# Kernel tuning notes

Measured on AMD Instinct MI355X. Metric: run time of the kernel, lower is better.

The kernel has to match this reference:

```python
import jax, jax.numpy as jnp
import numpy as np

N = 50000      # nodes
E = 800000     # edges
D = 128        # node feature dim
H = 128        # hid_channel (hardcoded in module)
B = 64         # graphs in batch
C = 3          # num_classes (COLLAB)
K = N // 2     # TopKPooling ratio=0.5


def setup_inputs() -> dict:
    key = jax.random.key(0)
    ks = jax.random.split(key, 16)
    s = 0.05
    return {
        "x": jax.random.normal(ks[0], (N, D), dtype=jnp.float32),
        "edge_index": jax.random.randint(ks[1], (E, 2), 0, N),
        "batch": jnp.sort(jax.random.randint(ks[2], (N,), 0, B)),
        "W1": jax.random.normal(ks[3], (D, H), dtype=jnp.float32) * s,
        "b1": jnp.zeros((H,), jnp.float32),
        "W2": jax.random.normal(ks[4], (H, H), dtype=jnp.float32) * s,
        "b2": jnp.zeros((H,), jnp.float32),
        "p": jax.random.normal(ks[5], (H,), dtype=jnp.float32),
        "W3": jax.random.normal(ks[6], (H, H), dtype=jnp.float32) * s,
        "b3": jnp.zeros((H,), jnp.float32),
        "W4": jax.random.normal(ks[7], (H, H), dtype=jnp.float32) * s,
        "b4": jnp.zeros((H,), jnp.float32),
        "fcW1": jax.random.normal(ks[8], (H, H), dtype=jnp.float32) * s,
        "fcb1": jnp.zeros((H,), jnp.float32),
        "fcW2": jax.random.normal(ks[9], (H, C), dtype=jnp.float32) * s,
        "fcb2": jnp.zeros((C,), jnp.float32),
    }


def gcn_conv(x, src, dst, ew, W, b, n):
    # PyG GCNConv: D^{-1/2}(A+I)D^{-1/2} x W + b, deg includes self-loop
    h = x @ W
    deg = jax.ops.segment_sum(ew, dst, num_segments=n) + 1.0
    dinv = jax.lax.rsqrt(deg)
    coef = dinv[src] * dinv[dst] * ew            # [E]
    agg = jax.ops.segment_sum(coef[:, None] * h[src], dst, num_segments=n)
    return agg + (dinv * dinv)[:, None] * h + b  # self-loop term + bias


def reference(x, edge_index, batch, W1, b1, W2, b2, p, W3, b3, W4, b4, fcW1, fcb1, fcW2, fcb2):
    src, dst = edge_index[:, 0], edge_index[:, 1]
    ew = jnp.ones((E,), x.dtype)

    h = jax.nn.relu(gcn_conv(x, src, dst, ew, W1, b1, N))
    h = jax.nn.relu(gcn_conv(h, src, dst, ew, W2, b2, N))

    # TopKPooling: score = x.p/||p||, keep top K, gate by tanh(score)
    score = h @ p / jnp.linalg.norm(p)
    top_vals, perm = jax.lax.top_k(score, K)
    hp = h[perm] * jnp.tanh(top_vals)[:, None]
    batch_p = batch[perm]
    new_idx = jnp.full((N,), -1, jnp.int32).at[perm].set(jnp.arange(K, dtype=jnp.int32))
    ns, nd = new_idx[src], new_idx[dst]
    mask = (ns >= 0) & (nd >= 0)
    ewp = mask.astype(x.dtype)
    ns = jnp.where(mask, ns, 0)
    nd = jnp.where(mask, nd, 0)

    h = jax.nn.relu(gcn_conv(hp, ns, nd, ewp, W3, b3, K))
    h = jax.nn.relu(gcn_conv(h, ns, nd, ewp, W4, b4, K))

    # global mean pool over graphs
    sums = jax.ops.segment_sum(h, batch_p, num_segments=B)
    cnt = jax.ops.segment_sum(jnp.ones((K,), x.dtype), batch_p, num_segments=B)
    g = sums / jnp.maximum(cnt, 1.0)[:, None]

    g = jax.nn.relu(g @ fcW1 + fcb1)
    logits = g @ fcW2 + fcb2
    return jax.nn.log_softmax(logits, axis=1)
```

## Files before the change

### kernel.cpp

```cpp
#include <hip/hip_runtime.h>

#define N_NODES 50000
#define N_EDGES 800000
#define HDIM    128
#define NBATCH  64
#define NCLS    3
#define KSEL    (N_NODES/2)
#define MMB_ROWS 64
#define HIST_BLOCKS 128
#define POOL_BLOCKS 256
#define POOL_CHUNK  ((KSEL + POOL_BLOCKS - 1) / POOL_BLOCKS)
#define NBUCK ((N_NODES + 127) >> 7)
#define EPB   2048
#define S1_BLOCKS ((N_EDGES + EPB - 1) / EPB)
#define SEG_CAP 4096

typedef unsigned long long u64;
typedef unsigned int u32;
typedef unsigned short ushort_t;
typedef _Float16 half8 __attribute__((ext_vector_type(8)));
typedef float floatx4 __attribute__((ext_vector_type(4)));

struct SelState { u64 prefix; int krem; int cnt; };

__device__ __forceinline__ float h2f(ushort_t u) {
    _Float16 h = *(_Float16*)&u;
    return (float)h;
}

__global__ void init_pnorm_k(const float* __restrict__ p, float* __restrict__ pn,
        SelState* st) {
    __shared__ float red[HDIM];
    int t = threadIdx.x;
    float v = p[t];
    red[t] = v * v;
    __syncthreads();
    for (int s = HDIM/2; s > 0; s >>= 1) {
        if (t < s) red[t] += red[t+s];
        __syncthreads();
    }
    pn[t] = v / sqrtf(red[0]);
    if (t == 0) { st->prefix = 0ull; st->krem = KSEL; st->cnt = 0; }
}

__global__ void deg_full_k(const int* __restrict__ ei, int* __restrict__ degi) {
    int e = blockIdx.x * blockDim.x + threadIdx.x;
    if (e >= N_EDGES) return;
    int2 ed = ((const int2*)ei)[e];
    atomicAdd(&degi[ed.y], 1);
}

__global__ __launch_bounds__(256) void scan12_k(const int* __restrict__ degi,
        int* __restrict__ bsum, int* __restrict__ boff, float* __restrict__ dinv,
        int* __restrict__ rowptr, int n, int nb, int* done) {
    __shared__ int sh[256];
    __shared__ int lastf;
    int t = threadIdx.x;
    int i = blockIdx.x * 256 + t;
    int d = (i < n) ? degi[i] : 0;
    if (i < n) dinv[i] = rsqrtf((float)d + 1.0f);
    sh[t] = d;
    __syncthreads();
    for (int s = 128; s > 0; s >>= 1) {
        if (t < s) sh[t] += sh[t + s];
        __syncthreads();
    }
    if (t == 0) {
        atomicExch(&bsum[blockIdx.x], sh[0]);
        __threadfence();
        int dd = atomicAdd(done, 1);
        lastf = (dd == (int)gridDim.x - 1) ? 1 : 0;
    }
    __syncthreads();
    if (lastf) {
        int v = (t < nb) ? atomicAdd(&bsum[t], 0) : 0;
        sh[t] = v;
        __syncthreads();
        for (int dl = 1; dl < 256; dl <<= 1) {
            int u = (t >= dl) ? sh[t - dl] : 0;
            __syncthreads();
            sh[t] += u;
            __syncthreads();
        }
        if (t < nb) boff[t] = sh[t] - v;
        if (t == 255) rowptr[n] = sh[255];
    }
}

__global__ __launch_bounds__(256) void scan3_k(const int* __restrict__ degi,
        const int* __restrict__ boff, int* __restrict__ rowptr, int n) {
    __shared__ int sh[256];
    int t = threadIdx.x;
    int i = blockIdx.x * 256 + t;
    int v = (i < n) ? degi[i] : 0;
    sh[t] = v;
    __syncthreads();
    for (int d = 1; d < 256; d <<= 1) {
        int u = (t >= d) ? sh[t - d] : 0;
        __syncthreads();
        sh[t] += u;
        __syncthreads();
    }
    if (i < n) rowptr[i] = boff[blockIdx.x] + sh[t] - v;
}

__global__ __launch_bounds__(256) void csr_bucket_k(const int* __restrict__ ei,
        const int* __restrict__ rowptr, u32* __restrict__ gcnt, u32* __restrict__ ebuf) {
    __shared__ u32 bh[NBUCK];
    __shared__ u32 cursor[NBUCK];
    int t = threadIdx.x;
    for (int i = t; i < NBUCK; i += 256) bh[i] = 0;
    __syncthreads();
    int e0 = blockIdx.x * EPB;
    int2 ed[8]; int nb[8];
#pragma unroll
    for (int i = 0; i < 8; ++i) {
        int e = e0 + t + i * 256;
        if (e < N_EDGES) {
            ed[i] = ((const int2*)ei)[e];
            nb[i] = ed[i].y >> 7;
            atomicAdd(&bh[nb[i]], 1u);
        } else nb[i] = -1;
    }
    __syncthreads();
    for (int b = t; b < NBUCK; b += 256) {
        u32 c = bh[b];
        if (c) cursor[b] = (u32)rowptr[b << 7] + atomicAdd(&gcnt[b], c);
    }
    __syncthreads();
#pragma unroll
    for (int i = 0; i < 8; ++i) {
        if (nb[i] >= 0) {
            u32 pos = atomicAdd(&cursor[nb[i]], 1u);
            ebuf[pos] = ((u32)(ed[i].y & 127) << 16) | (u32)ed[i].x;
        }
    }
}

__global__ __launch_bounds__(256) void csr_build_k(const u32* __restrict__ ebuf,
        const int* __restrict__ rowptr, int* __restrict__ csr) {
    __shared__ int rp[129];
    __shared__ int fcnt[128];
    __shared__ int seg[SEG_CAP];
    int b = blockIdx.x;
    int lo = b << 7;
    int nn = min(128, N_NODES - lo);
    int t = threadIdx.x;
    if (t <= nn) rp[t] = rowptr[lo + t];
    if (t < 128) fcnt[t] = 0;
    __syncthreads();
    int segbase = rp[0];
    int segsz = rp[nn] - segbase;
    if (segsz <= SEG_CAP) {
        for (int idx = t; idx < segsz; idx += 256) {
            u32 v = ebuf[segbase + idx];
            int dl = v >> 16;
            int slot = rp[dl] - segbase + atomicAdd(&fcnt[dl], 1);
            seg[slot] = (int)(v & 0xFFFFu);
        }
        __syncthreads();
        for (int idx = t; idx < segsz; idx += 256) csr[segbase + idx] = seg[idx];
    } else {
        for (int idx = t; idx < segsz; idx += 256) {
            u32 v = ebuf[segbase + idx];
            int dl = v >> 16;
            int slot = rp[dl] + atomicAdd(&fcnt[dl], 1);
            csr[slot] = (int)(v & 0xFFFFu);
        }
    }
}

__global__ __launch_bounds__(256) void gather_k(const int* __restrict__ rowptr,
        const int* __restrict__ csr, const float* __restrict__ dinv,
        const ushort_t* __restrict__ hb, const float* __restrict__ bias,
        float* __restrict__ out, int n) {
    int node = blockIdx.x * 4 + (threadIdx.x >> 6);
    if (node >= n) return;
    int lane = threadIdx.x & 63;
    float di = dinv[node];
    float2 bv = *(const float2*)&bias[2*lane];
    ushort2 hs = *(const ushort2*)&hb[(size_t)node * HDIM + 2*lane];
    float s2 = di * di;
    float accx = s2 * h2f(hs.x) + bv.x;
    float accy = s2 * h2f(hs.y) + bv.y;
    int rs = rowptr[node], re = rowptr[node + 1];
    for (int base = rs; base < re; base += 64) {
        int cnt = min(64, re - base);
        int srcv = 0; float cv = 0.0f;
        if (lane < cnt) { srcv = csr[base + lane]; cv = di * dinv[srcv]; }
        int j = 0;
        for (; j + 8 <= cnt; j += 8) {
            int s0 = __shfl(srcv, j+0, 64); int s1 = __shfl(srcv, j+1, 64);
            int s2i= __shfl(srcv, j+2, 64); int s3 = __shfl(srcv, j+3, 64);
            int s4 = __shfl(srcv, j+4, 64); int s5 = __shfl(srcv, j+5, 64);
            int s6 = __shfl(srcv, j+6, 64); int s7 = __shfl(srcv, j+7, 64);
            float c0 = __shfl(cv, j+0, 64); float c1 = __shfl(cv, j+1, 64);
            float c2 = __shfl(cv, j+2, 64); float c3 = __shfl(cv, j+3, 64);
            float c4 = __shfl(cv, j+4, 64); float c5 = __shfl(cv, j+5, 64);
            float c6 = __shfl(cv, j+6, 64); float c7 = __shfl(cv, j+7, 64);
            ushort2 v0 = *(const ushort2*)&hb[(size_t)s0 * HDIM + 2*lane];
            ushort2 v1 = *(const ushort2*)&hb[(size_t)s1 * HDIM + 2*lane];
            ushort2 v2 = *(const ushort2*)&hb[(size_t)s2i* HDIM + 2*lane];
            ushort2 v3 = *(const ushort2*)&hb[(size_t)s3 * HDIM + 2*lane];
            ushort2 v4 = *(const ushort2*)&hb[(size_t)s4 * HDIM + 2*lane];
            ushort2 v5 = *(const ushort2*)&hb[(size_t)s5 * HDIM + 2*lane];
            ushort2 v6 = *(const ushort2*)&hb[(size_t)s6 * HDIM + 2*lane];
            ushort2 v7 = *(const ushort2*)&hb[(size_t)s7 * HDIM + 2*lane];
            accx += c0*h2f(v0.x); accy += c0*h2f(v0.y);
            accx += c1*h2f(v1.x); accy += c1*h2f(v1.y);
            accx += c2*h2f(v2.x); accy += c2*h2f(v2.y);
            accx += c3*h2f(v3.x); accy += c3*h2f(v3.y);
            accx += c4*h2f(v4.x); accy += c4*h2f(v4.y);
            accx += c5*h2f(v5.x); accy += c5*h2f(v5.y);
            accx += c6*h2f(v6.x); accy += c6*h2f(v6.y);
            accx += c7*h2f(v7.x); accy += c7*h2f(v7.y);
        }
        for (; j < cnt; ++j) {
            int src = __shfl(srcv, j, 64);
            float c  = __shfl(cv, j, 64);
            ushort2 sv = *(const ushort2*)&hb[(size_t)src * HDIM + 2*lane];
            accx += c * h2f(sv.x);
            accy += c * h2f(sv.y);
        }
    }
    float2 o; o.x = accx; o.y = accy;
    *(float2*)&out[(size_t)node * HDIM + 2*lane] = o;
}

__global__ __launch_bounds__(256) void gather_pool_k(const int* __restrict__ rowptr,
        const int* __restrict__ csr, const int* __restrict__ n2o,
        const int2* __restrict__ pinfo, const float* __restrict__ dinvp,
        const ushort_t* __restrict__ hb, const float* __restrict__ bias,
        float* __restrict__ out) {
    __shared__ int   sns[4][64];
    __shared__ float scf[4][64];
    int k = blockIdx.x * 4 + (threadIdx.x >> 6);
    if (k >= KSEL) return;
    int wid = threadIdx.x >> 6, lane = threadIdx.x & 63;
    float di = dinvp[k];
    float2 bv = *(const float2*)&bias[2*lane];
    ushort2 hs = *(const ushort2*)&hb[(size_t)k * HDIM + 2*lane];
    float s2 = di * di;
    float accx = s2 * h2f(hs.x) + bv.x;
    float accy = s2 * h2f(hs.y) + bv.y;
    int old = n2o[k];
    int rs = rowptr[old], re = rowptr[old + 1];
    for (int base = rs; base < re; base += 64) {
        int span = min(64, re - base);
        int ns = -1; float dv = 0.0f;
        if (lane < span) {
            int2 pi = pinfo[csr[base + lane]];
            ns = pi.x; dv = __int_as_float(pi.y);
        }
        bool sel = (ns >= 0);
        u64 m = __ballot(sel);
        int rank = __popcll(m & ((1ull << lane) - 1ull));
        if (sel) { sns[wid][rank] = ns; scf[wid][rank] = di * dv; }
        int cnt = __popcll(m);
        __threadfence_block();
        int j = 0;
        for (; j + 8 <= cnt; j += 8) {
            int s0 = sns[wid][j+0]; int s1 = sns[wid][j+1];
            int s2i= sns[wid][j+2]; int s3 = sns[wid][j+3];
            int s4 = sns[wid][j+4]; int s5 = sns[wid][j+5];
            int s6 = sns[wid][j+6]; int s7 = sns[wid][j+7];
            float c0 = scf[wid][j+0]; float c1 = scf[wid][j+1];
            float c2 = scf[wid][j+2]; float c3 = scf[wid][j+3];
            float c4 = scf[wid][j+4]; float c5 = scf[wid][j+5];
            float c6 = scf[wid][j+6]; float c7 = scf[wid][j+7];
            ushort2 v0 = *(const ushort2*)&hb[(size_t)s0 * HDIM + 2*lane];
            ushort2 v1 = *(const ushort2*)&hb[(size_t)s1 * HDIM + 2*lane];
            ushort2 v2 = *(const ushort2*)&hb[(size_t)s2i* HDIM + 2*lane];
            ushort2 v3 = *(const ushort2*)&hb[(size_t)s3 * HDIM + 2*lane];
            ushort2 v4 = *(const ushort2*)&hb[(size_t)s4 * HDIM + 2*lane];
            ushort2 v5 = *(const ushort2*)&hb[(size_t)s5 * HDIM + 2*lane];
            ushort2 v6 = *(const ushort2*)&hb[(size_t)s6 * HDIM + 2*lane];
            ushort2 v7 = *(const ushort2*)&hb[(size_t)s7 * HDIM + 2*lane];
            accx += c0*h2f(v0.x); accy += c0*h2f(v0.y);
            accx += c1*h2f(v1.x); accy += c1*h2f(v1.y);
            accx += c2*h2f(v2.x); accy += c2*h2f(v2.y);
            accx += c3*h2f(v3.x); accy += c3*h2f(v3.y);
            accx += c4*h2f(v4.x); accy += c4*h2f(v4.y);
            accx += c5*h2f(v5.x); accy += c5*h2f(v5.y);
            accx += c6*h2f(v6.x); accy += c6*h2f(v6.y);
            accx += c7*h2f(v7.x); accy += c7*h2f(v7.y);
        }
        for (; j < cnt; ++j) {
            int src = sns[wid][j];
            float c = scf[wid][j];
            ushort2 sv = *(const ushort2*)&hb[(size_t)src * HDIM + 2*lane];
            accx += c * h2f(sv.x);
            accy += c * h2f(sv.y);
        }
    }
    float2 o; o.x = accx; o.y = accy;
    *(float2*)&out[(size_t)k * HDIM + 2*lane] = o;
}

template<bool RELU_IN>
__global__ __launch_bounds__(256) void matmul_k(const float* __restrict__ in,
        const float* __restrict__ W, ushort_t* __restrict__ outb, int rows) {
    __shared__ _Float16 Wf[4][8][64][8];
    int t = threadIdx.x;
    int rbase = blockIdx.x * MMB_ROWS;
    for (int idx = t; idx < HDIM * HDIM; idx += 256) {
        int k = idx >> 7, j = idx & 127;
        int kk = k >> 5, kgrp = (k >> 3) & 3, i = k & 7;
        int ct = j >> 4, lrow = j & 15;
        Wf[kk][ct][kgrp * 16 + lrow][i] = (_Float16)W[idx];
    }
    int wid = t >> 6, lane = t & 63;
    int lrow = lane & 15, kgrp = lane >> 4;
    int arow = rbase + wid * 16 + lrow;
    bool rowok = (arow < rows);
    const float* arp = in + (size_t)(rowok ? arow : 0) * HDIM + kgrp * 8;
    half8 a[4];
#pragma unroll
    for (int kk = 0; kk < 4; ++kk) {
        float4 lo = rowok ? *(const float4*)(arp + kk * 32)     : float4{0,0,0,0};
        float4 hi = rowok ? *(const float4*)(arp + kk * 32 + 4) : float4{0,0,0,0};
        if (RELU_IN) {
            lo.x = fmaxf(lo.x, 0.f); lo.y = fmaxf(lo.y, 0.f);
            lo.z = fmaxf(lo.z, 0.f); lo.w = fmaxf(lo.w, 0.f);
            hi.x = fmaxf(hi.x, 0.f); hi.y = fmaxf(hi.y, 0.f);
            hi.z = fmaxf(hi.z, 0.f); hi.w = fmaxf(hi.w, 0.f);
        }
        a[kk][0] = (_Float16)lo.x; a[kk][1] = (_Float16)lo.y;
        a[kk][2] = (_Float16)lo.z; a[kk][3] = (_Float16)lo.w;
        a[kk][4] = (_Float16)hi.x; a[kk][5] = (_Float16)hi.y;
        a[kk][6] = (_Float16)hi.z; a[kk][7] = (_Float16)hi.w;
    }
    __syncthreads();
    floatx4 zero4 = {0.0f, 0.0f, 0.0f, 0.0f};
    floatx4 acc[8];
#pragma unroll
    for (int ct = 0; ct < 8; ++ct) acc[ct] = zero4;
#pragma unroll
    for (int kk = 0; kk < 4; ++kk) {
#pragma unroll
        for (int ct = 0; ct < 8; ++ct) {
            half8 b = *(const half8*)&Wf[kk][ct][lane][0];
            acc[ct] = __builtin_amdgcn_mfma_f32_16x16x32_f16(a[kk], b, acc[ct], 0, 0, 0);
        }
    }
    int orow0 = rbase + wid * 16 + kgrp * 4;
#pragma unroll
    for (int ct = 0; ct < 8; ++ct) {
#pragma unroll
        for (int i = 0; i < 4; ++i) {
            int row = orow0 + i;
            if (row < rows) {
                _Float16 hv = (_Float16)acc[ct][i];
                outb[(size_t)row * HDIM + ct * 16 + lrow] = *(ushort_t*)&hv;
            }
        }
    }
}

__global__ void score_key_k(const float* __restrict__ h, const float* __restrict__ pn,
        float* __restrict__ score, u64* __restrict__ key) {
    int gid  = blockIdx.x * blockDim.x + threadIdx.x;
    int node = gid >> 6;
    int lane = gid & 63;
    if (node >= N_NODES) return;
    const float* row = h + (size_t)node * HDIM;
    float sv = fmaxf(row[lane], 0.f) * pn[lane] + fmaxf(row[lane+64], 0.f) * pn[lane+64];
#pragma unroll
    for (int o = 32; o > 0; o >>= 1) sv += __shfl_xor(sv, o, 64);
    if (lane == 0) {
        score[node] = sv;
        u32 u = __float_as_uint(sv);
        u = (u & 0x80000000u) ? ~u : (u | 0x80000000u);
        key[node] = ((u64)u << 16) | (u64)(65535 - node);
    }
}

__global__ __launch_bounds__(256) void histscan_k(const u64* __restrict__ key,
        SelState* st, u32* __restrict__ hist, int pass, int* done) {
    __shared__ u32 lh[256];
    __shared__ int lastf;
    int t = threadIdx.x;
    lh[t] = 0;
    __syncthreads();
    int dsh = 40 - 8 * pass;
    u64 pref = st->prefix;
    for (int i = blockIdx.x * 256 + t; i < N_NODES; i += HIST_BLOCKS * 256) {
        u64 k = key[i];
        if (((k ^ pref) >> (dsh + 8)) == 0)
            atomicAdd(&lh[(int)((k >> dsh) & 255)], 1u);
    }
    __syncthreads();
    u32 v = lh[t];
    if (v) atomicAdd(&hist[pass * 256 + t], v);
    __threadfence();
    __syncthreads();
    if (t == 0) {
        int dd = atomicAdd(done, 1);
        lastf = (dd == HIST_BLOCKS - 1) ? 1 : 0;
    }
    __syncthreads();
    if (lastf) {
        lh[t] = atomicAdd(&hist[pass * 256 + t], 0u);
        __syncthreads();
        if (t == 0) {
            int krem = st->krem;
            int b = 255;
            for (; b > 0; --b) {
                int cnt = (int)lh[b];
                if (cnt < krem) krem -= cnt;
                else break;
            }
            st->prefix |= ((u64)b) << dsh;
            st->krem = krem;
        }
    }
}

__global__ void select_k(const u64* __restrict__ key, SelState* st,
        int2* __restrict__ pinfo, int* __restrict__ n2o) {
    int i = blockIdx.x * blockDim.x + threadIdx.x;
    if (i >= N_NODES) return;
    if (key[i] >= st->prefix) {
        int pos = atomicAdd(&st->cnt, 1);
        pinfo[i].x = pos;
        n2o[pos] = i;
    } else {
        pinfo[i].x = -1;
    }
}

__global__ void hp_k(const float* __restrict__ h2, const float* __restrict__ score,
        const int* __restrict__ n2o, float* __restrict__ hp) {
    int gid = blockIdx.x * blockDim.x + threadIdx.x;
    if (gid >= KSEL * 32) return;
    int k  = gid >> 5;
    int c4 = (gid & 31) << 2;
    int old = n2o[k];
    float tv = tanhf(score[old]);
    float4 hv = *(const float4*)&h2[(size_t)old * HDIM + c4];
    float4 o;
    o.x = fmaxf(hv.x, 0.f) * tv;
    o.y = fmaxf(hv.y, 0.f) * tv;
    o.z = fmaxf(hv.z, 0.f) * tv;
    o.w = fmaxf(hv.w, 0.f) * tv;
    *(float4*)&hp[(size_t)k * HDIM + c4] = o;
}

__global__ __launch_bounds__(256) void pool_deg_k(const int* __restrict__ rowptr,
        const int* __restrict__ csr, const int* __restrict__ n2o,
        int2* __restrict__ pinfo, float* __restrict__ dinvp) {
    int k = blockIdx.x * 4 + (threadIdx.x >> 6);
    if (k >= KSEL) return;
    int lane = threadIdx.x & 63;
    int old = n2o[k];
    int rs = rowptr[old], re = rowptr[old + 1];
    int cnt = 0;
    for (int base = rs; base < re; base += 64) {
        int span = min(64, re - base);
        bool sel = false;
        if (lane < span) sel = (pinfo[csr[base + lane]].x >= 0);
        cnt += __popcll(__ballot(sel));
    }
    if (lane == 0) {
        float dv = rsqrtf((float)cnt + 1.0f);
        dinvp[k] = dv;
        pinfo[old].y = __float_as_int(dv);
    }
}

__global__ __launch_bounds__(256) void pool_stage1_k(const float* __restrict__ h,
        const int* __restrict__ n2o, const int* __restrict__ batch,
        float* __restrict__ partial, int* __restrict__ pcnt) {
    __shared__ float ls[NBATCH * HDIM];
    __shared__ int   lc[NBATCH];
    int t = threadIdx.x;
    for (int i = t; i < NBATCH * HDIM; i += 256) ls[i] = 0.0f;
    if (t < NBATCH) lc[t] = 0;
    __syncthreads();
    int wid = t >> 6, lane = t & 63;
    int start = blockIdx.x * POOL_CHUNK;
    int end = min(start + POOL_CHUNK, KSEL);
    for (int k = start + wid; k < end; k += 4) {
        int b = batch[n2o[k]];
        float2 hv = *(const float2*)&h[(size_t)k * HDIM + 2*lane];
        atomicAdd(&ls[b * HDIM + 2*lane],     fmaxf(hv.x, 0.0f));
        atomicAdd(&ls[b * HDIM + 2*lane + 1], fmaxf(hv.y, 0.0f));
        if (lane == 0) atomicAdd(&lc[b], 1);
    }
    __syncthreads();
    float* pb = partial + (size_t)blockIdx.x * (NBATCH * HDIM);
    for (int i = t; i < NBATCH * HDIM; i += 256) pb[i] = ls[i];
    if (t < NBATCH) pcnt[blockIdx.x * NBATCH + t] = lc[t];
}

__global__ __launch_bounds__(256) void pool_stage2_k(const float* __restrict__ partial,
        const int* __restrict__ pcnt, float* __restrict__ sums, float* __restrict__ cntb) {
    int i = blockIdx.x * 256 + threadIdx.x;
    if (i >= NBATCH * HDIM) return;
    float s = 0.0f;
    for (int p = 0; p < POOL_BLOCKS; ++p) s += partial[(size_t)p * NBATCH * HDIM + i];
    sums[i] = s;
    if (i < NBATCH) {
        int c = 0;
        for (int p = 0; p < POOL_BLOCKS; ++p) c += pcnt[p * NBATCH + i];
        cntb[i] = (float)c;
    }
}

__global__ void fc1_k(const float* __restrict__ sums, const float* __restrict__ cntb,
        const float* __restrict__ W, const float* __restrict__ bias, float* __restrict__ g) {
    int gid = blockIdx.x * blockDim.x + threadIdx.x;
    if (gid >= NBATCH * HDIM) return;
    int b = gid >> 7, j = gid & 127;
    float inv = 1.0f / fmaxf(cntb[b], 1.0f);
    float acc = 0.0f;
    for (int k = 0; k < HDIM; ++k) acc += sums[b * HDIM + k] * W[k * HDIM + j];
    acc = acc * inv + bias[j];
    g[gid] = fmaxf(acc, 0.0f);
}

__global__ void fc2_k(const float* __restrict__ g, const float* __restrict__ W,
        const float* __restrict__ bias, float* __restrict__ out) {
    int b = threadIdx.x;
    if (b >= NBATCH) return;
    float l[NCLS];
    for (int c = 0; c < NCLS; ++c) {
        float acc = bias[c];
        for (int k = 0; k < HDIM; ++k) acc += g[b * HDIM + k] * W[k * NCLS + c];
        l[c] = acc;
    }
    float m = fmaxf(l[0], fmaxf(l[1], l[2]));
    float sum = expf(l[0]-m) + expf(l[1]-m) + expf(l[2]-m);
    float ls = logf(sum);
    for (int c = 0; c < NCLS; ++c) out[b * NCLS + c] = l[c] - m - ls;
}

extern "C" void kernel_launch(void* const* d_in, const int* in_sizes, int n_in,
                              void* d_out, int out_size, void* d_ws, size_t ws_size,
                              hipStream_t stream) {
    const float* x    = (const float*)d_in[0];
    const int*   ei   = (const int*)d_in[1];
    const int*   batch= (const int*)d_in[2];
    const float* W1   = (const float*)d_in[3];
    const float* b1   = (const float*)d_in[4];
    const float* W2   = (const float*)d_in[5];
    const float* b2   = (const float*)d_in[6];
    const float* p    = (const float*)d_in[7];
    const float* W3   = (const float*)d_in[8];
    const float* b3   = (const float*)d_in[9];
    const float* W4   = (const float*)d_in[10];
    const float* b4   = (const float*)d_in[11];
    const float* fcW1 = (const float*)d_in[12];
    const float* fcb1 = (const float*)d_in[13];
    const float* fcW2 = (const float*)d_in[14];
    const float* fcb2 = (const float*)d_in[15];
    float* out = (float*)d_out;

    char* ws = (char*)d_ws;
    size_t off = 0;
    auto alloc = [&](size_t bytes) {
        size_t r = off;
        off = (off + bytes + 255) & ~(size_t)255;
        return r;
    };
    float* A     = (float*)(ws + alloc((size_t)N_NODES * HDIM * 4));
    float* Bf    = (float*)(ws + alloc((size_t)N_NODES * HDIM * 4));
    ushort_t* Hbf= (ushort_t*)(ws + alloc((size_t)N_NODES * HDIM * 2));
    u64*   key   = (u64*)  (ws + alloc((size_t)N_NODES * 8));
    float* score = (float*)(ws + alloc((size_t)N_NODES * 4));
    int2*  pinfo = (int2*) (ws + alloc((size_t)N_NODES * 8));
    int*   n2o   = (int*)  (ws + alloc((size_t)KSEL * 4));
    float* pn    = (float*)(ws + alloc(HDIM * 4));
    float* gbuf  = (float*)(ws + alloc(NBATCH * HDIM * 4));
    SelState* st = (SelState*)(ws + alloc(256));
    float* dinv1 = (float*)(ws + alloc((size_t)N_NODES * 4));
    float* dinvp = (float*)(ws + alloc((size_t)KSEL * 4));
    int*   rowptr= (int*)  (ws + alloc((size_t)(N_NODES + 1) * 4));
    int*   csr   = (int*)  (ws + alloc((size_t)N_EDGES * 4));
    u32*   ebuf  = (u32*)  (ws + alloc((size_t)N_EDGES * 4));
    int*   bsum  = (int*)  (ws + alloc(256 * 4));
    int*   boff  = (int*)  (ws + alloc(256 * 4));
    float* partial=(float*)(ws + alloc((size_t)POOL_BLOCKS * NBATCH * HDIM * 4));
    int*   pcnt  = (int*)  (ws + alloc((size_t)POOL_BLOCKS * NBATCH * 4));
    float* sums  = (float*)(ws + alloc(NBATCH * HDIM * 4));
    float* cntb  = (float*)(ws + alloc(NBATCH * 4));
    size_t z1 = off;
    int*   degi  = (int*)(ws + alloc((size_t)N_NODES * 4));
    u32*   gcnt  = (u32*)(ws + alloc((size_t)NBUCK * 4));
    u32*   hist  = (u32*)(ws + alloc(6 * 256 * 4));
    int*   done  = (int*)(ws + alloc(16 * 4));
    size_t z1e = off;

    hipMemsetAsync(ws + z1, 0, z1e - z1, stream);
    init_pnorm_k<<<1, HDIM, 0, stream>>>(p, pn, st);

    const int eg   = (N_EDGES + 255) / 256;
    const int ng   = (N_NODES + 255) / 256;
    const int mm_grid_n = (N_NODES + MMB_ROWS - 1) / MMB_ROWS;
    const int mm_grid_k = (KSEL + MMB_ROWS - 1) / MMB_ROWS;
    const int gt_grid_n = (N_NODES + 3) / 4;
    const int gt_grid_k = (KSEL + 3) / 4;
    const int kh4_grid  = (KSEL * 32 + 255) / 256;

    deg_full_k<<<eg, 256, 0, stream>>>(ei, degi);
    scan12_k<<<ng, 256, 0, stream>>>(degi, bsum, boff, dinv1, rowptr, N_NODES, ng, done + 0);
    scan3_k<<<ng, 256, 0, stream>>>(degi, boff, rowptr, N_NODES);
    csr_bucket_k<<<S1_BLOCKS, 256, 0, stream>>>(ei, rowptr, gcnt, ebuf);
    csr_build_k<<<NBUCK, 256, 0, stream>>>(ebuf, rowptr, csr);

    matmul_k<false><<<mm_grid_n, 256, 0, stream>>>(x, W1, Hbf, N_NODES);
    gather_k<<<gt_grid_n, 256, 0, stream>>>(rowptr, csr, dinv1, Hbf, b1, Bf, N_NODES);
    matmul_k<true><<<mm_grid_n, 256, 0, stream>>>(Bf, W2, Hbf, N_NODES);
    gather_k<<<gt_grid_n, 256, 0, stream>>>(rowptr, csr, dinv1, Hbf, b2, Bf, N_NODES);

    score_key_k<<<(N_NODES * 64 + 255) / 256, 256, 0, stream>>>(Bf, pn, score, key);
    for (int pass = 0; pass < 6; ++pass)
        histscan_k<<<HIST_BLOCKS, 256, 0, stream>>>(key, st, hist, pass, done + 2 + pass);
    select_k<<<ng, 256, 0, stream>>>(key, st, pinfo, n2o);
    hp_k<<<kh4_grid, 256, 0, stream>>>(Bf, score, n2o, A);

    pool_deg_k<<<gt_grid_k, 256, 0, stream>>>(rowptr, csr, n2o, pinfo, dinvp);

    matmul_k<false><<<mm_grid_k, 256, 0, stream>>>(A, W3, Hbf, KSEL);
    gather_pool_k<<<gt_grid_k, 256, 0, stream>>>(rowptr, csr, n2o, pinfo, dinvp, Hbf, b3, Bf);
    matmul_k<true><<<mm_grid_k, 256, 0, stream>>>(Bf, W4, Hbf, KSEL);
    gather_pool_k<<<gt_grid_k, 256, 0, stream>>>(rowptr, csr, n2o, pinfo, dinvp, Hbf, b4, A);

    pool_stage1_k<<<POOL_BLOCKS, 256, 0, stream>>>(A, n2o, batch, partial, pcnt);
    pool_stage2_k<<<(NBATCH * HDIM + 255) / 256, 256, 0, stream>>>(partial, pcnt, sums, cntb);
    fc1_k<<<(NBATCH * HDIM + 255) / 256, 256, 0, stream>>>(sums, cntb, fcW1, fcb1, gbuf);
    fc2_k<<<1, 64, 0, stream>>>(gbuf, fcW2, fcb2, out);
}
```

Measured before the change: 422.0 us.

## Fuse top-k selection pipeline into one persistent kernel with grid barriers

Replaces score, six radix histogram passes, select, hp gather and pooled-degree kernels with a single 128-block persistent kernel that uses atomic spin grid barriers between phases. The radix select now uses 12-bit digits over four passes, with a parallel prefix scan over the 4096-bin histogram. fc1 and fc2 are merged using a last-block-done pattern. This removes about ten kernel launches and their launch gaps. In exchange, the later phases run on only 128 blocks, and the spin barriers require every block to be co-resident on the GPU.

```diff
diff --git a/kernel.cpp b/kernel.cpp
--- a/kernel.cpp
+++ b/kernel.cpp
@@ -7,7 +7,7 @@
 #define NCLS    3
 #define KSEL    (N_NODES/2)
 #define MMB_ROWS 64
-#define HIST_BLOCKS 128
+#define TK_BLOCKS 128
 #define POOL_BLOCKS 256
 #define POOL_CHUNK  ((KSEL + POOL_BLOCKS - 1) / POOL_BLOCKS)
 #define NBUCK ((N_NODES + 127) >> 7)
@@ -357,114 +357,148 @@
     }
 }
 
-__global__ void score_key_k(const float* __restrict__ h, const float* __restrict__ pn,
-        float* __restrict__ score, u64* __restrict__ key) {
-    int gid  = blockIdx.x * blockDim.x + threadIdx.x;
-    int node = gid >> 6;
-    int lane = gid & 63;
-    if (node >= N_NODES) return;
-    const float* row = h + (size_t)node * HDIM;
-    float sv = fmaxf(row[lane], 0.f) * pn[lane] + fmaxf(row[lane+64], 0.f) * pn[lane+64];
-#pragma unroll
-    for (int o = 32; o > 0; o >>= 1) sv += __shfl_xor(sv, o, 64);
-    if (lane == 0) {
-        score[node] = sv;
-        u32 u = __float_as_uint(sv);
-        u = (u & 0x80000000u) ? ~u : (u | 0x80000000u);
-        key[node] = ((u64)u << 16) | (u64)(65535 - node);
-    }
-}
-
-__global__ __launch_bounds__(256) void histscan_k(const u64* __restrict__ key,
-        SelState* st, u32* __restrict__ hist, int pass, int* done) {
-    __shared__ u32 lh[256];
+__global__ __launch_bounds__(256) void topk_fused_k(const float* __restrict__ h,
+        const float* __restrict__ pn, float* __restrict__ score, u64* __restrict__ key,
+        SelState* st, u32* __restrict__ ghist, int* __restrict__ sync,
+        int2* __restrict__ pinfo, int* __restrict__ n2o,
+        const int* __restrict__ rowptr, const int* __restrict__ csr,
+        float* __restrict__ dinvp, float* __restrict__ hp) {
+    __shared__ u32 lh[4096];
+    __shared__ u32 sct[256];
+    __shared__ u64 spref;
+    __shared__ int skrem;
     __shared__ int lastf;
     int t = threadIdx.x;
-    lh[t] = 0;
-    __syncthreads();
-    int dsh = 40 - 8 * pass;
-    u64 pref = st->prefix;
-    for (int i = blockIdx.x * 256 + t; i < N_NODES; i += HIST_BLOCKS * 256) {
-        u64 k = key[i];
-        if (((k ^ pref) >> (dsh + 8)) == 0)
-            atomicAdd(&lh[(int)((k >> dsh) & 255)], 1u);
-    }
-    __syncthreads();
-    u32 v = lh[t];
-    if (v) atomicAdd(&hist[pass * 256 + t], v);
+    int lane = t & 63;
+    int gw = blockIdx.x * 4 + (t >> 6);
+
+    float pnl = pn[lane], pnh = pn[lane + 64];
+    for (int node = gw; node < N_NODES; node += TK_BLOCKS * 4) {
+        const float* row = h + (size_t)node * HDIM;
+        float sv = fmaxf(row[lane], 0.f) * pnl + fmaxf(row[lane+64], 0.f) * pnh;
+#pragma unroll
+        for (int o = 32; o > 0; o >>= 1) sv += __shfl_xor(sv, o, 64);
+        if (lane == 0) {
+            score[node] = sv;
+            u32 u = __float_as_uint(sv);
+            u = (u & 0x80000000u) ? ~u : (u | 0x80000000u);
+            key[node] = ((u64)u << 16) | (u64)(65535 - node);
+        }
+    }
+    __syncthreads();
+    if (t == 0) {
+        __threadfence();
+        int v = atomicAdd(&sync[10], 1);
+        if (v == TK_BLOCKS - 1) atomicExch(&sync[11], 1);
+        else while (atomicAdd(&sync[11], 0) == 0) __builtin_amdgcn_s_sleep(8);
+    }
+    __syncthreads();
     __threadfence();
+
+    for (int pass = 0; pass < 4; ++pass) {
+        int dsh = 36 - 12 * pass;
+        if (t == 0) spref = atomicAdd((unsigned long long*)&st->prefix, 0ull);
+        __syncthreads();
+        u64 pref = spref;
+        for (int b = t; b < 4096; b += 256) lh[b] = 0;
+        __syncthreads();
+        for (int i = blockIdx.x * 256 + t; i < N_NODES; i += TK_BLOCKS * 256) {
+            u64 k = key[i];
+            if (((k ^ pref) >> (dsh + 12)) == 0)
+                atomicAdd(&lh[(int)((k >> dsh) & 4095)], 1u);
+        }
+        __syncthreads();
+        for (int b = t; b < 4096; b += 256) {
+            u32 v = lh[b];
+            if (v) atomicAdd(&ghist[pass * 4096 + b], v);
+        }
+        __threadfence();
+        if (t == 0) {
+            int v = atomicAdd(&sync[2 + pass], 1);
+            lastf = (v == TK_BLOCKS - 1) ? 1 : 0;
+        }
+        __syncthreads();
+        if (lastf) {
+            for (int b = t; b < 4096; b += 256) lh[b] = atomicAdd(&ghist[pass * 4096 + b], 0u);
+            if (t == 0) skrem = atomicAdd(&st->krem, 0);
+            __syncthreads();
+            int krem = skrem;
+            u32 ctt = 0;
+#pragma unroll
+            for (int j = 0; j < 16; ++j) ctt += lh[t * 16 + j];
+            sct[t] = ctt;
+            __syncthreads();
+            for (int d = 1; d < 256; d <<= 1) {
+                u32 add = (t + d < 256) ? sct[t + d] : 0u;
+                __syncthreads();
+                sct[t] += add;
+                __syncthreads();
+            }
+            u32 incl = sct[t];
+            u32 excl = incl - ctt;
+            if ((int)excl < krem && (int)incl >= krem) {
+                u32 run = excl;
+                int bsel = 0; u32 csel = 0;
+                for (int j = 15; j >= 0; --j) {
+                    u32 c = lh[t * 16 + j];
+                    run += c;
+                    if ((int)run >= krem) { bsel = t * 16 + j; csel = c; break; }
+                }
+                int newk = krem - (int)(run - csel);
+                atomicExch((unsigned long long*)&st->prefix, spref | ((u64)bsel << dsh));
+                atomicExch(&st->krem, newk);
+            }
+            __syncthreads();
+            __threadfence();
+            if (t == 0) atomicExch(&sync[6 + pass], 1);
+        } else {
+            if (t == 0) while (atomicAdd(&sync[6 + pass], 0) == 0) __builtin_amdgcn_s_sleep(8);
+        }
+        __syncthreads();
+        __threadfence();
+    }
+
+    if (t == 0) spref = atomicAdd((unsigned long long*)&st->prefix, 0ull);
+    __syncthreads();
+    u64 pref = spref;
+    for (int i = blockIdx.x * 256 + t; i < N_NODES; i += TK_BLOCKS * 256) {
+        if (key[i] >= pref) {
+            int pos = atomicAdd(&st->cnt, 1);
+            pinfo[i].x = pos;
+            n2o[pos] = i;
+        } else {
+            pinfo[i].x = -1;
+        }
+    }
     __syncthreads();
     if (t == 0) {
-        int dd = atomicAdd(done, 1);
-        lastf = (dd == HIST_BLOCKS - 1) ? 1 : 0;
-    }
-    __syncthreads();
-    if (lastf) {
-        lh[t] = atomicAdd(&hist[pass * 256 + t], 0u);
-        __syncthreads();
-        if (t == 0) {
-            int krem = st->krem;
-            int b = 255;
-            for (; b > 0; --b) {
-                int cnt = (int)lh[b];
-                if (cnt < krem) krem -= cnt;
-                else break;
-            }
-            st->prefix |= ((u64)b) << dsh;
-            st->krem = krem;
-        }
-    }
-}
-
-__global__ void select_k(const u64* __restrict__ key, SelState* st,
-        int2* __restrict__ pinfo, int* __restrict__ n2o) {
-    int i = blockIdx.x * blockDim.x + threadIdx.x;
-    if (i >= N_NODES) return;
-    if (key[i] >= st->prefix) {
-        int pos = atomicAdd(&st->cnt, 1);
-        pinfo[i].x = pos;
-        n2o[pos] = i;
-    } else {
-        pinfo[i].x = -1;
-    }
-}
-
-__global__ void hp_k(const float* __restrict__ h2, const float* __restrict__ score,
-        const int* __restrict__ n2o, float* __restrict__ hp) {
-    int gid = blockIdx.x * blockDim.x + threadIdx.x;
-    if (gid >= KSEL * 32) return;
-    int k  = gid >> 5;
-    int c4 = (gid & 31) << 2;
-    int old = n2o[k];
-    float tv = tanhf(score[old]);
-    float4 hv = *(const float4*)&h2[(size_t)old * HDIM + c4];
-    float4 o;
-    o.x = fmaxf(hv.x, 0.f) * tv;
-    o.y = fmaxf(hv.y, 0.f) * tv;
-    o.z = fmaxf(hv.z, 0.f) * tv;
-    o.w = fmaxf(hv.w, 0.f) * tv;
-    *(float4*)&hp[(size_t)k * HDIM + c4] = o;
-}
-
-__global__ __launch_bounds__(256) void pool_deg_k(const int* __restrict__ rowptr,
-        const int* __restrict__ csr, const int* __restrict__ n2o,
-        int2* __restrict__ pinfo, float* __restrict__ dinvp) {
-    int k = blockIdx.x * 4 + (threadIdx.x >> 6);
-    if (k >= KSEL) return;
-    int lane = threadIdx.x & 63;
-    int old = n2o[k];
-    int rs = rowptr[old], re = rowptr[old + 1];
-    int cnt = 0;
-    for (int base = rs; base < re; base += 64) {
-        int span = min(64, re - base);
-        bool sel = false;
-        if (lane < span) sel = (pinfo[csr[base + lane]].x >= 0);
-        cnt += __popcll(__ballot(sel));
-    }
-    if (lane == 0) {
-        float dv = rsqrtf((float)cnt + 1.0f);
-        dinvp[k] = dv;
-        pinfo[old].y = __float_as_int(dv);
+        __threadfence();
+        int v = atomicAdd(&sync[12], 1);
+        if (v == TK_BLOCKS - 1) atomicExch(&sync[13], 1);
+        else while (atomicAdd(&sync[13], 0) == 0) __builtin_amdgcn_s_sleep(8);
+    }
+    __syncthreads();
+    __threadfence();
+
+    for (int k = gw; k < KSEL; k += TK_BLOCKS * 4) {
+        int old = n2o[k];
+        float tv = tanhf(score[old]);
+        const float* row = h + (size_t)old * HDIM;
+        hp[(size_t)k * HDIM + lane]      = fmaxf(row[lane], 0.f) * tv;
+        hp[(size_t)k * HDIM + lane + 64] = fmaxf(row[lane+64], 0.f) * tv;
+        int rs = rowptr[old], re = rowptr[old + 1];
+        int cnt = 0;
+        for (int base = rs; base < re; base += 64) {
+            int span = min(64, re - base);
+            bool sel = false;
+            if (lane < span) sel = (pinfo[csr[base + lane]].x >= 0);
+            cnt += __popcll(__ballot(sel));
+        }
+        if (lane == 0) {
+            float dv = rsqrtf((float)cnt + 1.0f);
+            dinvp[k] = dv;
+            pinfo[old].y = __float_as_int(dv);
+        }
     }
 }
 
@@ -507,26 +541,31 @@
     }
 }
 
-__global__ void fc1_k(const float* __restrict__ sums, const float* __restrict__ cntb,
-        const float* __restrict__ W, const float* __restrict__ bias, float* __restrict__ g) {
-    int gid = blockIdx.x * blockDim.x + threadIdx.x;
-    if (gid >= NBATCH * HDIM) return;
-    int b = gid >> 7, j = gid & 127;
-    float inv = 1.0f / fmaxf(cntb[b], 1.0f);
-    float acc = 0.0f;
-    for (int k = 0; k < HDIM; ++k) acc += sums[b * HDIM + k] * W[k * HDIM + j];
-    acc = acc * inv + bias[j];
-    g[gid] = fmaxf(acc, 0.0f);
-}
-
-__global__ void fc2_k(const float* __restrict__ g, const float* __restrict__ W,
-        const float* __restrict__ bias, float* __restrict__ out) {
-    int b = threadIdx.x;
-    if (b >= NBATCH) return;
+__global__ __launch_bounds__(256) void fc_k(const float* __restrict__ sums,
+        const float* __restrict__ cntb, const float* __restrict__ W1b,
+        const float* __restrict__ b1b, const float* __restrict__ W2b,
+        const float* __restrict__ b2b, float* __restrict__ gbuf,
+        float* __restrict__ out, int* done) {
+    int t = threadIdx.x;
+    int gid = blockIdx.x * 256 + t;
+    if (gid < NBATCH * HDIM) {
+        int b = gid >> 7, j = gid & 127;
+        float inv = 1.0f / fmaxf(cntb[b], 1.0f);
+        float acc = 0.0f;
+        for (int k = 0; k < HDIM; ++k) acc += sums[b * HDIM + k] * W1b[k * HDIM + j];
+        gbuf[gid] = fmaxf(acc * inv + b1b[j], 0.0f);
+    }
+    __threadfence();
+    __shared__ int lastf;
+    if (t == 0) lastf = (atomicAdd(done, 1) == (int)gridDim.x - 1) ? 1 : 0;
+    __syncthreads();
+    if (!lastf || t >= NBATCH) return;
+    __threadfence();
+    int b = t;
     float l[NCLS];
     for (int c = 0; c < NCLS; ++c) {
-        float acc = bias[c];
-        for (int k = 0; k < HDIM; ++k) acc += g[b * HDIM + k] * W[k * NCLS + c];
+        float acc = b2b[c];
+        for (int k = 0; k < HDIM; ++k) acc += gbuf[b * HDIM + k] * W2b[k * NCLS + c];
         l[c] = acc;
     }
     float m = fmaxf(l[0], fmaxf(l[1], l[2]));
@@ -587,8 +626,8 @@
     size_t z1 = off;
     int*   degi  = (int*)(ws + alloc((size_t)N_NODES * 4));
     u32*   gcnt  = (u32*)(ws + alloc((size_t)NBUCK * 4));
-    u32*   hist  = (u32*)(ws + alloc(6 * 256 * 4));
-    int*   done  = (int*)(ws + alloc(16 * 4));
+    u32*   ghist = (u32*)(ws + alloc(4 * 4096 * 4));
+    int*   sync  = (int*)(ws + alloc(32 * 4));
     size_t z1e = off;
 
     hipMemsetAsync(ws + z1, 0, z1e - z1, stream);
@@ -600,10 +639,9 @@
     const int mm_grid_k = (KSEL + MMB_ROWS - 1) / MMB_ROWS;
     const int gt_grid_n = (N_NODES + 3) / 4;
     const int gt_grid_k = (KSEL + 3) / 4;
-    const int kh4_grid  = (KSEL * 32 + 255) / 256;
 
     deg_full_k<<<eg, 256, 0, stream>>>(ei, degi);
-    scan12_k<<<ng, 256, 0, stream>>>(degi, bsum, boff, dinv1, rowptr, N_NODES, ng, done + 0);
+    scan12_k<<<ng, 256, 0, stream>>>(degi, bsum, boff, dinv1, rowptr, N_NODES, ng, sync + 0);
     scan3_k<<<ng, 256, 0, stream>>>(degi, boff, rowptr, N_NODES);
     csr_bucket_k<<<S1_BLOCKS, 256, 0, stream>>>(ei, rowptr, gcnt, ebuf);
     csr_build_k<<<NBUCK, 256, 0, stream>>>(ebuf, rowptr, csr);
@@ -613,13 +651,8 @@
     matmul_k<true><<<mm_grid_n, 256, 0, stream>>>(Bf, W2, Hbf, N_NODES);
     gather_k<<<gt_grid_n, 256, 0, stream>>>(rowptr, csr, dinv1, Hbf, b2, Bf, N_NODES);
 
-    score_key_k<<<(N_NODES * 64 + 255) / 256, 256, 0, stream>>>(Bf, pn, score, key);
-    for (int pass = 0; pass < 6; ++pass)
-        histscan_k<<<HIST_BLOCKS, 256, 0, stream>>>(key, st, hist, pass, done + 2 + pass);
-    select_k<<<ng, 256, 0, stream>>>(key, st, pinfo, n2o);
-    hp_k<<<kh4_grid, 256, 0, stream>>>(Bf, score, n2o, A);
-
-    pool_deg_k<<<gt_grid_k, 256, 0, stream>>>(rowptr, csr, n2o, pinfo, dinvp);
+    topk_fused_k<<<TK_BLOCKS, 256, 0, stream>>>(Bf, pn, score, key, st, ghist, sync,
+                                                pinfo, n2o, rowptr, csr, dinvp, A);
 
     matmul_k<false><<<mm_grid_k, 256, 0, stream>>>(A, W3, Hbf, KSEL);
     gather_pool_k<<<gt_grid_k, 256, 0, stream>>>(rowptr, csr, n2o, pinfo, dinvp, Hbf, b3, Bf);
@@ -628,6 +661,6 @@
 
     pool_stage1_k<<<POOL_BLOCKS, 256, 0, stream>>>(A, n2o, batch, partial, pcnt);
     pool_stage2_k<<<(NBATCH * HDIM + 255) / 256, 256, 0, stream>>>(partial, pcnt, sums, cntb);
-    fc1_k<<<(NBATCH * HDIM + 255) / 256, 256, 0, stream>>>(sums, cntb, fcW1, fcb1, gbuf);
-    fc2_k<<<1, 64, 0, stream>>>(gbuf, fcW2, fcb2, out);
-}
+    fc_k<<<(NBATCH * HDIM + 255) / 256, 256, 0, stream>>>(sums, cntb, fcW1, fcb1,
+                                                          fcW2, fcb2, gbuf, out, sync + 14);
+}
```

Result: slower. 548.9 us (+30.1%).
